# Kernel tuning notes

Hardware: AMD Instinct MI355X
Metric: run time of the kernel (lower is better)

## Reference

```python
import jax, jax.numpy as jnp
import numpy as np

B, T, C = 4, 2048, 1024
E, H, K = 8, 2048, 2


def setup_inputs() -> dict:
    key = jax.random.key(0)
    ks = jax.random.split(key, 7)
    s_in = 1.0 / np.sqrt(C)
    s_hid = 1.0 / np.sqrt(H)
    return {
        "x": jax.random.normal(ks[0], (B, T, C), dtype=jnp.float32),
        "gate_w": jax.random.uniform(ks[1], (C, E), jnp.float32, -s_in, s_in),
        "gate_b": jnp.zeros((E,), jnp.float32),
        "w1": jax.random.uniform(ks[2], (E, C, H), jnp.float32, -s_in, s_in),
        "b1": jax.random.uniform(ks[3], (E, H), jnp.float32, -s_in, s_in),
        "w2": jax.random.uniform(ks[4], (E, H, C), jnp.float32, -s_hid, s_hid),
        "b2": jax.random.uniform(ks[5], (E, C), jnp.float32, -s_hid, s_hid),
    }


def reference(x, gate_w, gate_b, w1, b1, w2, b2):
    b, t, c = x.shape
    xf = x.reshape(b * t, c)  # (N, C)

    # TopKGate: softmax over expert logits, take top-k gate values/indices
    logits = xf @ gate_w + gate_b              # (N, E)
    probs = jax.nn.softmax(logits, axis=-1)
    gates, expert_idx = jax.lax.top_k(probs, K)  # (N, K) each

    # Dense all-experts MLP (faithful to the original which runs every expert)
    h = jax.nn.relu(jnp.einsum('nc,ech->neh', xf, w1) + b1)  # (N, E, H)
    expert_out = jnp.einsum('neh,ehc->nec', h, w2) + b2      # (N, E, C)

    # Combine weights: scatter top-k gate values into (N, E), then weighted sum
    onehot = jax.nn.one_hot(expert_idx, E, dtype=xf.dtype)   # (N, K, E)
    weights = jnp.einsum('nk,nke->ne', gates, onehot)        # (N, E)
    out = jnp.einsum('ne,nec->nc', weights, expert_out)      # (N, C)
    return out.reshape(b, t, c)
```

## Files before the change

### kernel.cpp

```cpp
#include <hip/hip_runtime.h>
#include <cstdint>
#include <cstddef>

typedef __attribute__((ext_vector_type(8))) short short8;
typedef __attribute__((ext_vector_type(4))) float f32x4;
typedef __attribute__((ext_vector_type(4))) float flt4;

#define DEV __device__ __forceinline__

constexpr int C_ = 1024, E_ = 8, H_ = 2048, K_TOP = 2;
constexpr int N_ = 8192;
constexpr int NK_ = N_ * K_TOP;
constexpr int HB_ = 32;

DEV unsigned short f2bf(float f){
  unsigned u = __float_as_uint(f);
  u += 0x7fffu + ((u >> 16) & 1u);
  return (unsigned short)(u >> 16);
}

DEV void gload16(const void* g, void* l){
  __builtin_amdgcn_global_load_lds((const __attribute__((address_space(1))) unsigned int*)g,
                                   (__attribute__((address_space(3))) unsigned int*)l,
                                   16, 0, 0);
}

__global__ void cvt_x_kernel(const float* __restrict__ s, unsigned short* __restrict__ d){
  size_t i = ((size_t)blockIdx.x * blockDim.x + threadIdx.x) * 8;
  flt4 v0 = *(const flt4*)(s + i);
  flt4 v1 = *(const flt4*)(s + i + 4);
  short8 o;
  o[0]=f2bf(v0[0]); o[1]=f2bf(v0[1]); o[2]=f2bf(v0[2]); o[3]=f2bf(v0[3]);
  o[4]=f2bf(v1[0]); o[5]=f2bf(v1[1]); o[6]=f2bf(v1[2]); o[7]=f2bf(v1[3]);
  *(short8*)(d + i) = o;
}

__global__ void tconv_kernel(const float* __restrict__ src, unsigned short* __restrict__ dst,
                             int R, int S){
  __shared__ float tile[32][33];
  int e = blockIdx.z;
  int r0 = blockIdx.y * 32, s0 = blockIdx.x * 32;
  const float* se = src + (size_t)e * R * S;
  unsigned short* de = dst + (size_t)e * R * S;
  int tx = threadIdx.x & 31, ty = threadIdx.x >> 5;
  #pragma unroll
  for (int i = 0; i < 4; i++){
    int r = ty + i * 8;
    tile[r][tx] = se[(size_t)(r0 + r) * S + s0 + tx];
  }
  __syncthreads();
  #pragma unroll
  for (int i = 0; i < 4; i++){
    int s = ty + i * 8;
    de[(size_t)(s0 + s) * R + r0 + tx] = f2bf(tile[tx][s]);
  }
}

__global__ void gate_kernel(const float* __restrict__ x, const float* __restrict__ gw,
                            const float* __restrict__ gb,
                            int* __restrict__ tok_e, float* __restrict__ tok_g){
  int lane = threadIdx.x & 63;
  int n = blockIdx.x * 4 + (threadIdx.x >> 6);
  const float* xr = x + (size_t)n * C_;
  float acc[E_];
  #pragma unroll
  for (int e = 0; e < E_; e++) acc[e] = 0.f;
  #pragma unroll 4
  for (int j = 0; j < C_ / 64; j++){
    int c = lane + j * 64;
    float xv = xr[c];
    flt4 g0 = *(const flt4*)(gw + (size_t)c * E_);
    flt4 g1 = *(const flt4*)(gw + (size_t)c * E_ + 4);
    acc[0] += xv * g0[0]; acc[1] += xv * g0[1]; acc[2] += xv * g0[2]; acc[3] += xv * g0[3];
    acc[4] += xv * g1[0]; acc[5] += xv * g1[1]; acc[6] += xv * g1[2]; acc[7] += xv * g1[3];
  }
  #pragma unroll
  for (int e = 0; e < E_; e++)
    #pragma unroll
    for (int off = 32; off > 0; off >>= 1)
      acc[e] += __shfl_xor(acc[e], off, 64);
  if (lane == 0){
    float l[E_], p[E_];
    float m = -1e30f;
    #pragma unroll
    for (int e = 0; e < E_; e++){ l[e] = acc[e] + gb[e]; m = fmaxf(m, l[e]); }
    float s = 0.f;
    #pragma unroll
    for (int e = 0; e < E_; e++){ p[e] = expf(l[e] - m); s += p[e]; }
    float inv = 1.f / s;
    int e0 = 0; float m0 = p[0];
    #pragma unroll
    for (int e = 1; e < E_; e++) if (p[e] > m0){ m0 = p[e]; e0 = e; }
    int e1 = -1; float m1 = -1.f;
    #pragma unroll
    for (int e = 0; e < E_; e++) if (e != e0 && p[e] > m1){ m1 = p[e]; e1 = e; }
    tok_e[2*n]   = e0; tok_g[2*n]   = m0 * inv;
    tok_e[2*n+1] = e1; tok_g[2*n+1] = m1 * inv;
  }
}

__global__ void hist_kernel(const int* __restrict__ tok_e, int* __restrict__ blockhist){
  __shared__ int h[E_];
  if (threadIdx.x < E_) h[threadIdx.x] = 0;
  __syncthreads();
  int n = blockIdx.x * 256 + threadIdx.x;
  int e0 = tok_e[2*n], e1 = tok_e[2*n+1];
  atomicAdd(&h[e0], 1);
  atomicAdd(&h[e1], 1);
  __syncthreads();
  if (threadIdx.x < E_) blockhist[blockIdx.x * E_ + threadIdx.x] = h[threadIdx.x];
}

__global__ void scan2_kernel(const int* __restrict__ blockhist, int* __restrict__ counts,
                             int* __restrict__ offsets, int* __restrict__ blockbase){
  if (threadIdx.x == 0){
    int tot[E_];
    for (int e = 0; e < E_; e++){
      int s = 0;
      for (int b = 0; b < HB_; b++) s += blockhist[b * E_ + e];
      tot[e] = s;
    }
    int s = 0;
    for (int e = 0; e < E_; e++){ counts[e] = tot[e]; offsets[e] = s; s += tot[e]; }
    for (int e = 0; e < E_; e++){
      int cur = offsets[e];
      for (int b = 0; b < HB_; b++){ blockbase[b * E_ + e] = cur; cur += blockhist[b * E_ + e]; }
    }
  }
}

__global__ void build_kernel(const int* __restrict__ tok_e, const float* __restrict__ tok_g,
                             const int* __restrict__ blockbase,
                             int* __restrict__ list_tok, float* __restrict__ list_gate){
  __shared__ int cur[E_];
  if (threadIdx.x < E_) cur[threadIdx.x] = blockbase[blockIdx.x * E_ + threadIdx.x];
  __syncthreads();
  int n = blockIdx.x * 256 + threadIdx.x;
  #pragma unroll
  for (int k = 0; k < K_TOP; k++){
    int e = tok_e[2*n + k];
    int pos = atomicAdd(&cur[e], 1);
    list_tok[pos] = n;
    list_gate[pos] = tok_g[2*n + k];
  }
}

template<bool FIRST>
__global__ __launch_bounds__(512, 4)
void moe_gemm(const unsigned short* __restrict__ Abase,
              const unsigned short* __restrict__ Bbase,
              const float* __restrict__ bias,
              const int* __restrict__ counts, const int* __restrict__ offsets,
              const int* __restrict__ list_tok, const float* __restrict__ list_gate,
              unsigned short* __restrict__ hbuf, float* __restrict__ out){
  constexpr int K   = FIRST ? C_ : H_;
  constexpr int ND  = FIRST ? H_ : C_;
  constexpr int GX  = ND / 128;
  constexpr int LGX = FIRST ? 4 : 3;
  constexpr int GY  = N_ / 128;
  __shared__ unsigned char smem[32768];

  int lin  = blockIdx.x + GX * (blockIdx.y + GY * blockIdx.z);
  int work = (lin & 7) * (GX * GY) + (lin >> 3);
  int bx = work & (GX - 1);
  int by = (work >> LGX) & (GY - 1);
  int e  = work >> (LGX + 6);

  int ne = counts[e];
  int row0 = by * 128;
  if (row0 >= ne) return;
  int off = offsets[e];
  int col0 = bx * 128;
  int tid = threadIdx.x;
  int lane = tid & 63, wave = tid >> 6;
  int wm = wave >> 2, wn = wave & 3;
  int lr = lane & 15, lk = lane >> 4;
  int rr = tid >> 3;
  int chunk = (tid & 7) ^ (rr & 7);

  const unsigned short* Bexp = Bbase + (size_t)e * ND * K;
  const unsigned short* agsrc[2];
  const unsigned short* bgsrc[2];
  #pragma unroll
  for (int j = 0; j < 2; j++){
    int r = j * 64 + rr;
    int rc = min(row0 + r, ne - 1);
    size_t arow = FIRST ? (size_t)list_tok[off + rc] * C_ : (size_t)(off + rc) * H_;
    agsrc[j] = Abase + arow + chunk * 8;
    bgsrc[j] = Bexp + (size_t)(col0 + r) * K + chunk * 8;
  }
  unsigned char* Adst = smem + wave * 1024;
  unsigned char* Bdst = smem + 16384 + wave * 1024;

  f32x4 acc[4][2];
  #pragma unroll
  for (int a = 0; a < 4; a++)
    #pragma unroll
    for (int b = 0; b < 2; b++) acc[a][b] = (f32x4){0.f,0.f,0.f,0.f};

  for (int k0 = 0; k0 < K; k0 += 64){
    __syncthreads();
    #pragma unroll
    for (int j = 0; j < 2; j++) gload16(agsrc[j] + k0, Adst + j * 8192);
    #pragma unroll
    for (int j = 0; j < 2; j++) gload16(bgsrc[j] + k0, Bdst + j * 8192);
    __syncthreads();
    #pragma unroll
    for (int s = 0; s < 2; s++){
      short8 av[4], bv[2];
      int kx = ((s * 4 + lk) ^ (lr & 7)) * 16;
      #pragma unroll
      for (int fm = 0; fm < 4; fm++){
        int row = wm * 64 + fm * 16 + lr;
        av[fm] = *(const short8*)(smem + row * 128 + kx);
      }
      #pragma unroll
      for (int fn = 0; fn < 2; fn++){
        int col = wn * 32 + fn * 16 + lr;
        bv[fn] = *(const short8*)(smem + 16384 + col * 128 + kx);
      }
      #pragma unroll
      for (int fm = 0; fm < 4; fm++)
        #pragma unroll
        for (int fn = 0; fn < 2; fn++)
          acc[fm][fn] = __builtin_amdgcn_mfma_f32_16x16x32_bf16(av[fm], bv[fn], acc[fm][fn], 0, 0, 0);
    }
  }

  if (FIRST){
    #pragma unroll
    for (int fm = 0; fm < 4; fm++){
      int rbase = row0 + wm*64 + fm*16 + lk*4;
      #pragma unroll
      for (int fn = 0; fn < 2; fn++){
        int colb = col0 + wn*32 + fn*16 + lr;
        float bv2 = bias[e*ND + colb];
        #pragma unroll
        for (int i = 0; i < 4; i++){
          int r = rbase + i;
          if (r < ne){
            float v = acc[fm][fn][i] + bv2;
            v = v > 0.f ? v : 0.f;
            hbuf[(size_t)(off + r)*H_ + colb] = f2bf(v);
          }
        }
      }
    }
  } else {
    #pragma unroll
    for (int fm = 0; fm < 4; fm++){
      int rbase = row0 + wm*64 + fm*16 + lk*4;
      #pragma unroll
      for (int i = 0; i < 4; i++){
        int r = rbase + i;
        if (r < ne){
          int pos = off + r;
          int tok = list_tok[pos];
          float g = list_gate[pos];
          float* orow = out + (size_t)tok * C_;
          #pragma unroll
          for (int fn = 0; fn < 2; fn++){
            int colb = col0 + wn*32 + fn*16 + lr;
            float v = (acc[fm][fn][i] + bias[e*ND + colb]) * g;
            atomicAdd(orow + colb, v);
          }
        }
      }
    }
  }
}

extern "C" void kernel_launch(void* const* d_in, const int* in_sizes, int n_in,
                              void* d_out, int out_size, void* d_ws, size_t ws_size,
                              hipStream_t stream){
  const float* x  = (const float*)d_in[0];
  const float* gw = (const float*)d_in[1];
  const float* gb = (const float*)d_in[2];
  const float* w1 = (const float*)d_in[3];
  const float* b1 = (const float*)d_in[4];
  const float* w2 = (const float*)d_in[5];
  const float* b2 = (const float*)d_in[6];
  float* out = (float*)d_out;

  char* p = (char*)d_ws;
  unsigned short* xb   = (unsigned short*)p; p += (size_t)N_*C_*2;
  unsigned short* w1t  = (unsigned short*)p; p += (size_t)E_*C_*H_*2;
  unsigned short* w2t  = (unsigned short*)p; p += (size_t)E_*C_*H_*2;
  unsigned short* hbuf = (unsigned short*)p; p += (size_t)NK_*H_*2;
  int*   tok_e     = (int*)p;   p += (size_t)NK_*4;
  float* tok_g     = (float*)p; p += (size_t)NK_*4;
  int*   list_tok  = (int*)p;   p += (size_t)NK_*4;
  float* list_gate = (float*)p; p += (size_t)NK_*4;
  int*   counts    = (int*)p;   p += 256;
  int*   offsets   = (int*)p;   p += 256;
  int*   blockhist = (int*)p;   p += HB_*E_*4;
  int*   blockbase = (int*)p;   p += HB_*E_*4;

  hipMemsetAsync(out, 0, (size_t)out_size * sizeof(float), stream);

  cvt_x_kernel<<<(N_*C_/8)/256, 256, 0, stream>>>(x, xb);
  tconv_kernel<<<dim3(H_/32, C_/32, E_), 256, 0, stream>>>(w1, w1t, C_, H_);
  tconv_kernel<<<dim3(C_/32, H_/32, E_), 256, 0, stream>>>(w2, w2t, H_, C_);
  gate_kernel<<<N_/4, 256, 0, stream>>>(x, gw, gb, tok_e, tok_g);
  hist_kernel<<<HB_, 256, 0, stream>>>(tok_e, blockhist);
  scan2_kernel<<<1, 64, 0, stream>>>(blockhist, counts, offsets, blockbase);
  build_kernel<<<HB_, 256, 0, stream>>>(tok_e, tok_g, blockbase, list_tok, list_gate);

  moe_gemm<true ><<<dim3(H_/128, N_/128, E_), 512, 0, stream>>>(xb,   w1t, b1, counts, offsets, list_tok, list_gate, hbuf, out);
  moe_gemm<false><<<dim3(C_/128, N_/128, E_), 512, 0, stream>>>(hbuf, w2t, b2, counts, offsets, list_tok, list_gate, hbuf, out);
}
```

Baseline: 349.8 us.

## Pipeline MoE GEMM K-loop with four-stage async LDS buffering

Replaces the single-buffer load/sync/compute loop with a four-slot LDS ring, issuing global-to-LDS loads three tiles ahead and using explicit vmcnt waits plus one barrier per iteration. The aim is to hide global memory latency behind MFMA work and remove one of the two barriers per K step. In exchange it uses 128KB of LDS per block and lowers launch bounds to 2 blocks per CU, which reduces occupancy. The hand-written waitcnt sequencing also risks subtle correctness problems if the compiler reorders memory operations.

```diff
diff --git a/kernel.cpp b/kernel.cpp
--- a/kernel.cpp
+++ b/kernel.cpp
@@ -146,7 +146,7 @@
 }
 
 template<bool FIRST>
-__global__ __launch_bounds__(512, 4)
+__global__ __launch_bounds__(512, 2)
 void moe_gemm(const unsigned short* __restrict__ Abase,
               const unsigned short* __restrict__ Bbase,
               const float* __restrict__ bias,
@@ -154,11 +154,12 @@
               const int* __restrict__ list_tok, const float* __restrict__ list_gate,
               unsigned short* __restrict__ hbuf, float* __restrict__ out){
   constexpr int K   = FIRST ? C_ : H_;
+  constexpr int NT  = K / 64;
   constexpr int ND  = FIRST ? H_ : C_;
   constexpr int GX  = ND / 128;
   constexpr int LGX = FIRST ? 4 : 3;
   constexpr int GY  = N_ / 128;
-  __shared__ unsigned char smem[32768];
+  __shared__ unsigned char smem[131072];
 
   int lin  = blockIdx.x + GX * (blockIdx.y + GY * blockIdx.z);
   int work = (lin & 7) * (GX * GY) + (lin >> 3);
@@ -189,8 +190,7 @@
     agsrc[j] = Abase + arow + chunk * 8;
     bgsrc[j] = Bexp + (size_t)(col0 + r) * K + chunk * 8;
   }
-  unsigned char* Adst = smem + wave * 1024;
-  unsigned char* Bdst = smem + 16384 + wave * 1024;
+  unsigned char* dstW = smem + wave * 1024;
 
   f32x4 acc[4][2];
   #pragma unroll
@@ -198,13 +198,24 @@
     #pragma unroll
     for (int b = 0; b < 2; b++) acc[a][b] = (f32x4){0.f,0.f,0.f,0.f};
 
-  for (int k0 = 0; k0 < K; k0 += 64){
-    __syncthreads();
-    #pragma unroll
-    for (int j = 0; j < 2; j++) gload16(agsrc[j] + k0, Adst + j * 8192);
-    #pragma unroll
-    for (int j = 0; j < 2; j++) gload16(bgsrc[j] + k0, Bdst + j * 8192);
-    __syncthreads();
+  #define STAGE(t) do{                                              \
+    int _b = ((t) & 3) * 32768;                                     \
+    int _kn = (t) * 64;                                             \
+    gload16(agsrc[0] + _kn, dstW + _b + 0);                         \
+    gload16(agsrc[1] + _kn, dstW + _b + 8192);                      \
+    gload16(bgsrc[0] + _kn, dstW + _b + 16384);                     \
+    gload16(bgsrc[1] + _kn, dstW + _b + 16384 + 8192);              \
+  }while(0)
+
+  STAGE(0); STAGE(1); STAGE(2);
+  asm volatile("s_waitcnt vmcnt(8)" ::: "memory");
+  __builtin_amdgcn_s_barrier();
+  __builtin_amdgcn_sched_barrier(0);
+
+  for (int t = 0; t < NT; ++t){
+    if (t + 3 < NT) STAGE(t + 3);
+    const unsigned char* Ab = smem + (t & 3) * 32768;
+    const unsigned char* Bb = Ab + 16384;
     #pragma unroll
     for (int s = 0; s < 2; s++){
       short8 av[4], bv[2];
@@ -212,12 +223,12 @@
       #pragma unroll
       for (int fm = 0; fm < 4; fm++){
         int row = wm * 64 + fm * 16 + lr;
-        av[fm] = *(const short8*)(smem + row * 128 + kx);
+        av[fm] = *(const short8*)(Ab + row * 128 + kx);
       }
       #pragma unroll
       for (int fn = 0; fn < 2; fn++){
         int col = wn * 32 + fn * 16 + lr;
-        bv[fn] = *(const short8*)(smem + 16384 + col * 128 + kx);
+        bv[fn] = *(const short8*)(Bb + col * 128 + kx);
       }
       #pragma unroll
       for (int fm = 0; fm < 4; fm++)
@@ -225,7 +236,13 @@
         for (int fn = 0; fn < 2; fn++)
           acc[fm][fn] = __builtin_amdgcn_mfma_f32_16x16x32_bf16(av[fm], bv[fn], acc[fm][fn], 0, 0, 0);
     }
-  }
+    if (t + 3 < NT)      asm volatile("s_waitcnt vmcnt(8)" ::: "memory");
+    else if (t + 2 < NT) asm volatile("s_waitcnt vmcnt(4)" ::: "memory");
+    else if (t + 1 < NT) asm volatile("s_waitcnt vmcnt(0)" ::: "memory");
+    __builtin_amdgcn_s_barrier();
+    __builtin_amdgcn_sched_barrier(0);
+  }
+  #undef STAGE
 
   if (FIRST){
     #pragma unroll
```

Measured after the change: 401.0 us. 14.6% more time.
